# Kernel tuning notes

Measured on AMD Instinct MI355X. Metric: run time of the kernel, lower is better.

Reference implementation:

```python
import jax, jax.numpy as jnp
import numpy as np

jax.config.update("jax_enable_x64", True)  # hash arithmetic needs 64-bit ints

P = 56598313          # RzLinear.P (prime for the hash)
INPUT_DIM = 4096
OUTPUT_DIM = 4096
COMPRESS_RATIO = 0.0625
HASH_SIZE = int(INPUT_DIM * OUTPUT_DIM * COMPRESS_RATIO)  # 1,048,576
N_TOKENS = 8192


def setup_inputs() -> dict:
    key = jax.random.key(0)
    kx, kw, kr = jax.random.split(key, 3)
    x = jax.random.normal(kx, (N_TOKENS, INPUT_DIM), dtype=jnp.float32)
    hashed_weight = jax.random.normal(kw, (HASH_SIZE,), dtype=jnp.float32) * 0.02
    # _generate_random_numbers: [P, r1, r2, r3] with r_i forced even via r + r % 2
    r = jax.random.randint(kr, (3,), 0, P, dtype=jnp.int64)
    r = r + r % 2
    random_numbers = jnp.concatenate([jnp.array([P], dtype=jnp.int64), r])
    bias = jnp.zeros((OUTPUT_DIM,), dtype=jnp.float32)
    return {"x": x, "hashed_weight": hashed_weight,
            "random_numbers": random_numbers, "bias": bias}


def _hash_indices(random_numbers):
    # ROBE-Z hash (chunk_size=1): idx[k, n] = ((k*r3 + n*r2 + r1) % P) % HASH_SIZE
    r0 = random_numbers[0]
    r1 = random_numbers[1]
    r2 = random_numbers[2]
    r3 = random_numbers[3]
    k = jnp.arange(INPUT_DIM, dtype=jnp.int64)[:, None]   # (K, 1)
    n = jnp.arange(OUTPUT_DIM, dtype=jnp.int64)[None, :]  # (1, N)
    return ((k * r3 + n * r2 + r1) % r0) % HASH_SIZE       # (K, N)


def reference(x, hashed_weight, random_numbers, bias):
    idx = _hash_indices(random_numbers)
    W = hashed_weight[idx]          # gather-reconstructed (input_dim, output_dim)
    return x @ W + bias             # (N_TOKENS, output_dim)
```

## Files before the change

kernel.cpp:

```cpp
#include <hip/hip_runtime.h>
#include <stdint.h>


#define P_CONST 56598313u
#define HASH_MASK 0xFFFFFu
#define M_DIM 8192
#define N_DIM 4096
#define K_DIM 4096
#define BK 32
#define KSTEPS (K_DIM / BK)

typedef __attribute__((ext_vector_type(8))) short bf16x8;
typedef __attribute__((ext_vector_type(4))) float f32x4;

__device__ __forceinline__ unsigned short f2bf(float f) {
    unsigned int u = __float_as_uint(f);
    return (unsigned short)((u + 0x7FFFu + ((u >> 16) & 1u)) >> 16);
}

struct RN { unsigned long long r1, r2, r3; };

__device__ __forceinline__ RN decode_rn(const void* rn_raw) {
    RN o;
    const long long* rn64 = (const long long*)rn_raw;
    if (rn64[0] == 56598313LL) {
        o.r1 = (unsigned long long)rn64[1];
        o.r2 = (unsigned long long)rn64[2];
        o.r3 = (unsigned long long)rn64[3];
    } else {
        const int* rn32 = (const int*)rn_raw;
        o.r1 = (unsigned long long)(unsigned int)rn32[1];
        o.r2 = (unsigned long long)(unsigned int)rn32[2];
        o.r3 = (unsigned long long)(unsigned int)rn32[3];
    }
    return o;
}

__device__ __forceinline__ void load16(const void* g, void* l) {
    __builtin_amdgcn_global_load_lds(
        (const __attribute__((address_space(1))) void*)g,
        (__attribute__((address_space(3))) void*)l,
        16, 0, 0);
}

__global__ __launch_bounds__(256) void build_wt(const float* __restrict__ table,
                                                const void* __restrict__ rn_raw,
                                                unsigned short* __restrict__ Wt) {
    RN rn = decode_rn(rn_raw);
    const unsigned int stepu = (unsigned int)(rn.r3 % P_CONST);
    const unsigned int n = blockIdx.x;
    const unsigned long long base =
        ((unsigned long long)n * rn.r2 + rn.r1) % P_CONST;
    const int t = threadIdx.x;
#pragma unroll
    for (int e = 0; e < 2; ++e) {
        const int k0 = (t + e * 256) * 8;
        unsigned int cur =
            (unsigned int)((base + (unsigned long long)k0 * stepu) % P_CONST);
        union { unsigned short s[8]; uint4 v; } o;
#pragma unroll
        for (int i = 0; i < 8; ++i) {
            o.s[i] = f2bf(table[cur & HASH_MASK]);
            cur += stepu;
            if (cur >= P_CONST) cur -= P_CONST;
        }
        *(uint4*)(Wt + (size_t)n * K_DIM + k0) = o.v;
    }
}

__global__ __launch_bounds__(256) void cvt_x(const float* __restrict__ x,
                                             unsigned short* __restrict__ xb) {
    const size_t i8 = ((size_t)blockIdx.x * 256 + threadIdx.x) * 8;
    const float4 a = *(const float4*)(x + i8);
    const float4 b = *(const float4*)(x + i8 + 4);
    union { unsigned short s[8]; uint4 v; } o;
    o.s[0] = f2bf(a.x); o.s[1] = f2bf(a.y); o.s[2] = f2bf(a.z); o.s[3] = f2bf(a.w);
    o.s[4] = f2bf(b.x); o.s[5] = f2bf(b.y); o.s[6] = f2bf(b.z); o.s[7] = f2bf(b.w);
    *(uint4*)(xb + i8) = o.v;
}

__global__ __launch_bounds__(512, 2) void gemm_bt8(
    const unsigned short* __restrict__ A,
    const unsigned short* __restrict__ Bt,
    const float* __restrict__ bias,
    float* __restrict__ C) {
    __shared__ __align__(16) unsigned short lA[4][256 * BK];
    __shared__ __align__(16) unsigned short lB[4][256 * BK];

    const int t = threadIdx.x;
    const int bid0 = blockIdx.x;
    const int sb = (bid0 & 7) * 64 + (bid0 >> 3);
    const int m0 = (sb >> 4) * 256;
    const int n0 = (sb & 15) * 256;

    const int lane = t & 63;
    const int wid = t >> 6;
    const int wr = wid >> 2;
    const int wc = wid & 3;
    const int lm = lane & 15;
    const int q = lane >> 4;
    const int qswz = (q ^ ((lm >> 1) & 3)) << 4;

    const int p0 = t * 16;
    const int p1 = p0 + 8192;
    const int l0 = p0 ^ ((p0 >> 3) & 0x30);
    const int l1 = p1 ^ ((p1 >> 3) & 0x30);
    const int r0 = l0 >> 6, c0 = (l0 & 63) >> 1;
    const int r1 = l1 >> 6, c1 = (l1 & 63) >> 1;

    const unsigned short* Abase = A + (size_t)m0 * K_DIM;
    const unsigned short* Bbase = Bt + (size_t)n0 * K_DIM;

    f32x4 acc[8][4] = {};

#define STAGE_A(KS) do { const int b__ = (KS) & 3;                              \
    load16(Abase + (size_t)r0 * K_DIM + (KS) * BK + c0, (char*)&lA[b__][0] + p0);\
    load16(Abase + (size_t)r1 * K_DIM + (KS) * BK + c1, (char*)&lA[b__][0] + p1);\
} while (0)
#define STAGE_B(KS) do { const int b__ = (KS) & 3;                              \
    load16(Bbase + (size_t)r0 * K_DIM + (KS) * BK + c0, (char*)&lB[b__][0] + p0);\
    load16(Bbase + (size_t)r1 * K_DIM + (KS) * BK + c1, (char*)&lB[b__][0] + p1);\
} while (0)

#define STEP_BODY(KS, STG) do {                                                 \
    __builtin_amdgcn_s_barrier();                                               \
    asm volatile("" ::: "memory");                                              \
    const char* bufA = (const char*)&lA[(KS) & 3][0];                           \
    const char* bufB = (const char*)&lB[(KS) & 3][0];                           \
    bf16x8 af[4], bfr[4];                                                       \
    _Pragma("unroll")                                                           \
    for (int i = 0; i < 4; ++i)                                                 \
        af[i] = *(const bf16x8*)(bufA + (((wr * 128 + i * 16 + lm) << 6) | qswz));\
    _Pragma("unroll")                                                           \
    for (int j = 0; j < 4; ++j)                                                 \
        bfr[j] = *(const bf16x8*)(bufB + (((wc * 64 + j * 16 + lm) << 6) | qswz));\
    if (STG) STAGE_A((KS) + 3);                                                 \
    asm volatile("s_waitcnt lgkmcnt(0)" ::: "memory");                          \
    __builtin_amdgcn_sched_barrier(0);                                          \
    __builtin_amdgcn_s_setprio(1);                                              \
    _Pragma("unroll")                                                           \
    for (int i = 0; i < 4; ++i)                                                 \
        _Pragma("unroll")                                                       \
        for (int j = 0; j < 4; ++j)                                             \
            acc[i][j] = __builtin_amdgcn_mfma_f32_16x16x32_bf16(                \
                af[i], bfr[j], acc[i][j], 0, 0, 0);                             \
    __builtin_amdgcn_s_setprio(0);                                              \
    __builtin_amdgcn_s_barrier();                                               \
    asm volatile("" ::: "memory");                                              \
    _Pragma("unroll")                                                           \
    for (int i = 0; i < 4; ++i)                                                 \
        af[i] = *(const bf16x8*)(bufA + (((wr * 128 + 64 + i * 16 + lm) << 6) | qswz));\
    if (STG) STAGE_B((KS) + 3);                                                 \
    asm volatile("s_waitcnt lgkmcnt(0)" ::: "memory");                          \
    __builtin_amdgcn_sched_barrier(0);                                          \
    __builtin_amdgcn_s_setprio(1);                                              \
    _Pragma("unroll")                                                           \
    for (int i = 0; i < 4; ++i)                                                 \
        _Pragma("unroll")                                                       \
        for (int j = 0; j < 4; ++j)                                             \
            acc[i + 4][j] = __builtin_amdgcn_mfma_f32_16x16x32_bf16(            \
                af[i], bfr[j], acc[i + 4][j], 0, 0, 0);                         \
    __builtin_amdgcn_s_setprio(0);                                              \
} while (0)

    STAGE_A(0); STAGE_B(0);
    STAGE_A(1); STAGE_B(1);
    STAGE_A(2); STAGE_B(2);

#pragma unroll 1
    for (int ks = 0; ks < KSTEPS - 2; ++ks) {
        asm volatile("s_waitcnt vmcnt(8)" ::: "memory");
        STEP_BODY(ks, (ks < KSTEPS - 3));
    }
    asm volatile("s_waitcnt vmcnt(4)" ::: "memory");
    STEP_BODY(KSTEPS - 2, false);
    asm volatile("s_waitcnt vmcnt(0)" ::: "memory");
    STEP_BODY(KSTEPS - 1, false);

#undef STEP_BODY
#undef STAGE_A
#undef STAGE_B

#pragma unroll
    for (int j = 0; j < 4; ++j) {
        const int col = n0 + wc * 64 + j * 16 + lm;
        const float bv = bias[col];
#pragma unroll
        for (int i = 0; i < 8; ++i) {
            const int row = m0 + wr * 128 + i * 16 + q * 4;
#pragma unroll
            for (int r = 0; r < 4; ++r)
                C[(size_t)(row + r) * N_DIM + col] = acc[i][j][r] + bv;
        }
    }
}

__global__ __launch_bounds__(256) void gemm_fused(const float* __restrict__ X,
                                                  const float* __restrict__ table,
                                                  const void* __restrict__ rn_raw,
                                                  const float* __restrict__ bias,
                                                  float* __restrict__ C) {
    RN rn = decode_rn(rn_raw);
    const unsigned int stepu = (unsigned int)(rn.r3 % P_CONST);
    const unsigned int step32 =
        (unsigned int)(((unsigned long long)stepu * 32ull) % P_CONST);

    __shared__ __align__(16) unsigned short lA[128 * 32];
    __shared__ __align__(16) unsigned short lB[128 * 32];
    const int t = threadIdx.x;
    const int m0 = blockIdx.y * 128;
    const int n0 = blockIdx.x * 128;
    const int lane = t & 63;
    const int w = t >> 6;
    const int wr = w >> 1, wc = w & 1;
    const int lm = lane & 15, q = lane >> 4;

    unsigned int curB[2];
    int rowB[2], colB[2];
#pragma unroll
    for (int e = 0; e < 2; ++e) {
        const int c = t + e * 256;
        rowB[e] = c >> 2;
        colB[e] = (c & 3) * 8;
        const unsigned long long base =
            ((unsigned long long)(n0 + rowB[e]) * rn.r2 + rn.r1) % P_CONST;
        curB[e] =
            (unsigned int)((base + (unsigned long long)colB[e] * stepu) % P_CONST);
    }

    f32x4 acc[4][4] = {};

    for (int k0 = 0; k0 < K_DIM; k0 += 32) {
#pragma unroll
        for (int c = t; c < 1024; c += 256) {
            const int row = c >> 3, col = (c & 7) * 4;
            const float4 v =
                *(const float4*)(X + (size_t)(m0 + row) * K_DIM + k0 + col);
            ushort4 o;
            o.x = f2bf(v.x); o.y = f2bf(v.y); o.z = f2bf(v.z); o.w = f2bf(v.w);
            *(ushort4*)&lA[row * 32 + col] = o;
        }
#pragma unroll
        for (int e = 0; e < 2; ++e) {
            unsigned int cur = curB[e];
            union { unsigned short s[8]; uint4 v; } o;
#pragma unroll
            for (int i = 0; i < 8; ++i) {
                o.s[i] = f2bf(table[cur & HASH_MASK]);
                cur += stepu;
                if (cur >= P_CONST) cur -= P_CONST;
            }
            curB[e] += step32;
            if (curB[e] >= P_CONST) curB[e] -= P_CONST;
            *(uint4*)&lB[rowB[e] * 32 + colB[e]] = o.v;
        }
        __syncthreads();

        bf16x8 af[4], bfr[4];
#pragma unroll
        for (int i = 0; i < 4; ++i)
            af[i] = *(const bf16x8*)&lA[(wr * 64 + i * 16 + lm) * 32 + q * 8];
#pragma unroll
        for (int j = 0; j < 4; ++j)
            bfr[j] = *(const bf16x8*)&lB[(wc * 64 + j * 16 + lm) * 32 + q * 8];
#pragma unroll
        for (int i = 0; i < 4; ++i)
#pragma unroll
            for (int j = 0; j < 4; ++j)
                acc[i][j] = __builtin_amdgcn_mfma_f32_16x16x32_bf16(
                    af[i], bfr[j], acc[i][j], 0, 0, 0);
        __syncthreads();
    }

#pragma unroll
    for (int j = 0; j < 4; ++j) {
        const int col = n0 + wc * 64 + j * 16 + lm;
        const float bv = bias[col];
#pragma unroll
        for (int i = 0; i < 4; ++i) {
            const int row = m0 + wr * 64 + i * 16 + q * 4;
#pragma unroll
            for (int r = 0; r < 4; ++r)
                C[(size_t)(row + r) * N_DIM + col] = acc[i][j][r] + bv;
        }
    }
}

extern "C" void kernel_launch(void* const* d_in, const int* in_sizes, int n_in,
                              void* d_out, int out_size, void* d_ws, size_t ws_size,
                              hipStream_t stream) {
    const float* x = (const float*)d_in[0];
    const float* hw = (const float*)d_in[1];
    const void* rn = d_in[2];
    const float* bias = (const float*)d_in[3];
    float* out = (float*)d_out;

    const size_t wt_bytes = (size_t)N_DIM * K_DIM * 2;
    const size_t xb_bytes = (size_t)M_DIM * K_DIM * 2;

    if (ws_size >= wt_bytes + xb_bytes) {
        unsigned short* Wt = (unsigned short*)d_ws;
        unsigned short* Xb = (unsigned short*)((char*)d_ws + wt_bytes);
        build_wt<<<N_DIM, 256, 0, stream>>>(hw, rn, Wt);
        cvt_x<<<(M_DIM * K_DIM) / (8 * 256), 256, 0, stream>>>(x, Xb);
        gemm_bt8<<<dim3((M_DIM / 256) * (N_DIM / 256)), 512, 0, stream>>>(Xb, Wt, bias, out);
    } else {
        gemm_fused<<<dim3(N_DIM / 128, M_DIM / 128), 256, 0, stream>>>(x, hw, rn, bias, out);
    }
}
```

Measured before the change: 534.7 us.

## Fuse weight gather with x conversion and pre-convert hash table to bf16

The hash table is converted to bf16 once, which halves its footprint so it stays cache-resident. The weight-gather kernel and the x-to-bf16 conversion are merged into one launch, with each thread gathering four weight entries and converting eight x values. The streaming x reads and the Xb/Wt writes use nontemporal hints. This adds one small kernel and extra workspace, and falls back to an fp32-table fused prep when the workspace is too small.

```diff
diff --git a/kernel.cpp b/kernel.cpp
--- a/kernel.cpp
+++ b/kernel.cpp
@@ -12,6 +12,8 @@
 
 typedef __attribute__((ext_vector_type(8))) short bf16x8;
 typedef __attribute__((ext_vector_type(4))) float f32x4;
+typedef __attribute__((ext_vector_type(4))) unsigned int u32x4;
+typedef __attribute__((ext_vector_type(2))) unsigned int u32x2;
 
 __device__ __forceinline__ unsigned short f2bf(float f) {
     unsigned int u = __float_as_uint(f);
@@ -43,40 +45,87 @@
         16, 0, 0);
 }
 
-__global__ __launch_bounds__(256) void build_wt(const float* __restrict__ table,
-                                                const void* __restrict__ rn_raw,
-                                                unsigned short* __restrict__ Wt) {
+__global__ __launch_bounds__(256) void cvt_tbl(const float* __restrict__ table,
+                                               unsigned short* __restrict__ tb) {
+    const size_t i8 = ((size_t)blockIdx.x * 256 + threadIdx.x) * 8;
+    const f32x4 a = *(const f32x4*)(table + i8);
+    const f32x4 c = *(const f32x4*)(table + i8 + 4);
+    union { unsigned short s[8]; u32x4 v; } o;
+    o.s[0] = f2bf(a.x); o.s[1] = f2bf(a.y); o.s[2] = f2bf(a.z); o.s[3] = f2bf(a.w);
+    o.s[4] = f2bf(c.x); o.s[5] = f2bf(c.y); o.s[6] = f2bf(c.z); o.s[7] = f2bf(c.w);
+    *(u32x4*)(tb + i8) = o.v;
+}
+
+__global__ __launch_bounds__(256) void prep_bf(const float* __restrict__ x,
+                                               const unsigned short* __restrict__ tb,
+                                               const void* __restrict__ rn_raw,
+                                               unsigned short* __restrict__ Wt,
+                                               unsigned short* __restrict__ Xb) {
+    const int b = blockIdx.x;
+    const int t = threadIdx.x;
     RN rn = decode_rn(rn_raw);
     const unsigned int stepu = (unsigned int)(rn.r3 % P_CONST);
-    const unsigned int n = blockIdx.x;
+    const unsigned int n = (unsigned int)(b >> 2);
+    const int kb = ((b & 3) << 10) + (t << 2);
     const unsigned long long base =
         ((unsigned long long)n * rn.r2 + rn.r1) % P_CONST;
+    unsigned int cur =
+        (unsigned int)((base + (unsigned long long)kb * stepu) % P_CONST);
+    const unsigned int i0 = cur & HASH_MASK;
+    cur += stepu; if (cur >= P_CONST) cur -= P_CONST;
+    const unsigned int i1 = cur & HASH_MASK;
+    cur += stepu; if (cur >= P_CONST) cur -= P_CONST;
+    const unsigned int i2 = cur & HASH_MASK;
+    cur += stepu; if (cur >= P_CONST) cur -= P_CONST;
+    const unsigned int i3 = cur & HASH_MASK;
+    const unsigned short g0 = tb[i0];
+    const unsigned short g1 = tb[i1];
+    const unsigned short g2 = tb[i2];
+    const unsigned short g3 = tb[i3];
+    const size_t i8 = ((size_t)b * 256 + t) * 8;
+    const f32x4 a = __builtin_nontemporal_load((const f32x4*)(x + i8));
+    const f32x4 c = __builtin_nontemporal_load((const f32x4*)(x + i8 + 4));
+    union { unsigned short s[8]; u32x4 v; } o;
+    o.s[0] = f2bf(a.x); o.s[1] = f2bf(a.y); o.s[2] = f2bf(a.z); o.s[3] = f2bf(a.w);
+    o.s[4] = f2bf(c.x); o.s[5] = f2bf(c.y); o.s[6] = f2bf(c.z); o.s[7] = f2bf(c.w);
+    __builtin_nontemporal_store(o.v, (u32x4*)(Xb + i8));
+    union { unsigned short s[4]; u32x2 v; } w;
+    w.s[0] = g0; w.s[1] = g1; w.s[2] = g2; w.s[3] = g3;
+    __builtin_nontemporal_store(w.v, (u32x2*)(Wt + (size_t)n * K_DIM + kb));
+}
+
+__global__ __launch_bounds__(256) void prep_f32(const float* __restrict__ x,
+                                                const float* __restrict__ table,
+                                                const void* __restrict__ rn_raw,
+                                                unsigned short* __restrict__ Wt,
+                                                unsigned short* __restrict__ Xb) {
+    const int b = blockIdx.x;
     const int t = threadIdx.x;
-#pragma unroll
-    for (int e = 0; e < 2; ++e) {
-        const int k0 = (t + e * 256) * 8;
-        unsigned int cur =
-            (unsigned int)((base + (unsigned long long)k0 * stepu) % P_CONST);
-        union { unsigned short s[8]; uint4 v; } o;
-#pragma unroll
-        for (int i = 0; i < 8; ++i) {
-            o.s[i] = f2bf(table[cur & HASH_MASK]);
-            cur += stepu;
-            if (cur >= P_CONST) cur -= P_CONST;
-        }
-        *(uint4*)(Wt + (size_t)n * K_DIM + k0) = o.v;
-    }
-}
-
-__global__ __launch_bounds__(256) void cvt_x(const float* __restrict__ x,
-                                             unsigned short* __restrict__ xb) {
-    const size_t i8 = ((size_t)blockIdx.x * 256 + threadIdx.x) * 8;
-    const float4 a = *(const float4*)(x + i8);
-    const float4 b = *(const float4*)(x + i8 + 4);
-    union { unsigned short s[8]; uint4 v; } o;
+    RN rn = decode_rn(rn_raw);
+    const unsigned int stepu = (unsigned int)(rn.r3 % P_CONST);
+    const unsigned int n = (unsigned int)(b >> 2);
+    const int kb = ((b & 3) << 10) + (t << 2);
+    const unsigned long long base =
+        ((unsigned long long)n * rn.r2 + rn.r1) % P_CONST;
+    unsigned int cur =
+        (unsigned int)((base + (unsigned long long)kb * stepu) % P_CONST);
+    const float g0 = table[cur & HASH_MASK];
+    cur += stepu; if (cur >= P_CONST) cur -= P_CONST;
+    const float g1 = table[cur & HASH_MASK];
+    cur += stepu; if (cur >= P_CONST) cur -= P_CONST;
+    const float g2 = table[cur & HASH_MASK];
+    cur += stepu; if (cur >= P_CONST) cur -= P_CONST;
+    const float g3 = table[cur & HASH_MASK];
+    const size_t i8 = ((size_t)b * 256 + t) * 8;
+    const f32x4 a = __builtin_nontemporal_load((const f32x4*)(x + i8));
+    const f32x4 c = __builtin_nontemporal_load((const f32x4*)(x + i8 + 4));
+    union { unsigned short s[8]; u32x4 v; } o;
     o.s[0] = f2bf(a.x); o.s[1] = f2bf(a.y); o.s[2] = f2bf(a.z); o.s[3] = f2bf(a.w);
-    o.s[4] = f2bf(b.x); o.s[5] = f2bf(b.y); o.s[6] = f2bf(b.z); o.s[7] = f2bf(b.w);
-    *(uint4*)(xb + i8) = o.v;
+    o.s[4] = f2bf(c.x); o.s[5] = f2bf(c.y); o.s[6] = f2bf(c.z); o.s[7] = f2bf(c.w);
+    __builtin_nontemporal_store(o.v, (u32x4*)(Xb + i8));
+    union { unsigned short s[4]; u32x2 v; } w;
+    w.s[0] = f2bf(g0); w.s[1] = f2bf(g1); w.s[2] = f2bf(g2); w.s[3] = f2bf(g3);
+    __builtin_nontemporal_store(w.v, (u32x2*)(Wt + (size_t)n * K_DIM + kb));
 }
 
 __global__ __launch_bounds__(512, 2) void gemm_bt8(
@@ -297,12 +346,19 @@
 
     const size_t wt_bytes = (size_t)N_DIM * K_DIM * 2;
     const size_t xb_bytes = (size_t)M_DIM * K_DIM * 2;
-
-    if (ws_size >= wt_bytes + xb_bytes) {
+    const size_t tb_bytes = (size_t)(HASH_MASK + 1) * 2;
+
+    if (ws_size >= wt_bytes + xb_bytes + tb_bytes) {
         unsigned short* Wt = (unsigned short*)d_ws;
         unsigned short* Xb = (unsigned short*)((char*)d_ws + wt_bytes);
-        build_wt<<<N_DIM, 256, 0, stream>>>(hw, rn, Wt);
-        cvt_x<<<(M_DIM * K_DIM) / (8 * 256), 256, 0, stream>>>(x, Xb);
+        unsigned short* Tb = (unsigned short*)((char*)d_ws + wt_bytes + xb_bytes);
+        cvt_tbl<<<512, 256, 0, stream>>>(hw, Tb);
+        prep_bf<<<16384, 256, 0, stream>>>(x, Tb, rn, Wt, Xb);
+        gemm_bt8<<<dim3((M_DIM / 256) * (N_DIM / 256)), 512, 0, stream>>>(Xb, Wt, bias, out);
+    } else if (ws_size >= wt_bytes + xb_bytes) {
+        unsigned short* Wt = (unsigned short*)d_ws;
+        unsigned short* Xb = (unsigned short*)((char*)d_ws + wt_bytes);
+        prep_f32<<<16384, 256, 0, stream>>>(x, hw, rn, Wt, Xb);
         gemm_bt8<<<dim3((M_DIM / 256) * (N_DIM / 256)), 512, 0, stream>>>(Xb, Wt, bias, out);
     } else {
         gemm_fused<<<dim3(N_DIM / 128, M_DIM / 128), 256, 0, stream>>>(x, hw, rn, bias, out);
```

Result: slower. 571.1 us (+6.8%).

## Build hashed weight via bf16 table staged through LDS shards

Applied to the files above, without the earlier changes.

Converts the hash table to bf16 once, then rebuilds the weight matrix with 1024-thread blocks that stream the table through a 128KB LDS buffer in 16 shards. Each thread gathers its entries from LDS and keeps only those whose index falls in the current shard. This replaces random global-memory gathers with coalesced loads plus LDS lookups. In exchange it adds an extra kernel launch and redundant per-shard hash and LDS work, and the single large-LDS block per CU limits occupancy.

```diff
diff --git a/kernel.cpp b/kernel.cpp
--- a/kernel.cpp
+++ b/kernel.cpp
@@ -12,6 +12,7 @@
 
 typedef __attribute__((ext_vector_type(8))) short bf16x8;
 typedef __attribute__((ext_vector_type(4))) float f32x4;
+typedef __attribute__((ext_vector_type(4))) unsigned int u32x4;
 
 __device__ __forceinline__ unsigned short f2bf(float f) {
     unsigned int u = __float_as_uint(f);
@@ -43,6 +44,78 @@
         16, 0, 0);
 }
 
+__global__ __launch_bounds__(256) void cvt_tbl(const float* __restrict__ table,
+                                               unsigned short* __restrict__ tb) {
+    const size_t i8 = ((size_t)blockIdx.x * 256 + threadIdx.x) * 8;
+    const f32x4 a = *(const f32x4*)(table + i8);
+    const f32x4 c = *(const f32x4*)(table + i8 + 4);
+    union { unsigned short s[8]; u32x4 v; } o;
+    o.s[0] = f2bf(a.x); o.s[1] = f2bf(a.y); o.s[2] = f2bf(a.z); o.s[3] = f2bf(a.w);
+    o.s[4] = f2bf(c.x); o.s[5] = f2bf(c.y); o.s[6] = f2bf(c.z); o.s[7] = f2bf(c.w);
+    *(u32x4*)(tb + i8) = o.v;
+}
+
+__global__ __launch_bounds__(1024) void build_wt_lds(
+    const unsigned short* __restrict__ tb,
+    const void* __restrict__ rn_raw,
+    unsigned short* __restrict__ Wt) {
+    __shared__ __align__(16) unsigned short shard[65536];
+    RN rn = decode_rn(rn_raw);
+    const unsigned int stepu = (unsigned int)(rn.r3 % P_CONST);
+    const unsigned int jump504 =
+        (unsigned int)((504ull * stepu) % P_CONST);
+    const int b = blockIdx.x;
+    const int t = threadIdx.x;
+    const unsigned int n = (unsigned int)(b * 16 + (t >> 6));
+    const int kbase = (t & 63) * 8;
+    const unsigned long long base =
+        ((unsigned long long)n * rn.r2 + rn.r1) % P_CONST;
+    const unsigned int cur0 =
+        (unsigned int)((base + (unsigned long long)kbase * stepu) % P_CONST);
+
+    bf16x8 wv[8] = {};
+
+#pragma unroll 1
+    for (int s = 0; s < 16; ++s) {
+        __syncthreads();
+#pragma unroll
+        for (int i = 0; i < 8; ++i)
+            load16(tb + ((size_t)s << 16) + (i << 13) + t * 8,
+                   (char*)shard + (i << 14) + t * 16);
+        asm volatile("s_waitcnt vmcnt(0)" ::: "memory");
+        __syncthreads();
+
+        unsigned int cur = cur0;
+#pragma unroll
+        for (int j = 0; j < 8; ++j) {
+#pragma unroll
+            for (int i = 0; i < 8; ++i) {
+                const unsigned int idx = cur & HASH_MASK;
+                const unsigned short v = shard[idx & 0xFFFFu];
+                if ((idx >> 16) == (unsigned int)s) wv[j][i] = (short)v;
+                cur += stepu; if (cur >= P_CONST) cur -= P_CONST;
+            }
+            cur += jump504; if (cur >= P_CONST) cur -= P_CONST;
+        }
+    }
+
+    unsigned short* dst = Wt + (size_t)n * K_DIM + kbase;
+#pragma unroll
+    for (int j = 0; j < 8; ++j)
+        *(bf16x8*)(dst + j * 512) = wv[j];
+}
+
+__global__ __launch_bounds__(256) void cvt_x(const float* __restrict__ x,
+                                             unsigned short* __restrict__ xb) {
+    const size_t i8 = ((size_t)blockIdx.x * 256 + threadIdx.x) * 8;
+    const f32x4 a = *(const f32x4*)(x + i8);
+    const f32x4 c = *(const f32x4*)(x + i8 + 4);
+    union { unsigned short s[8]; u32x4 v; } o;
+    o.s[0] = f2bf(a.x); o.s[1] = f2bf(a.y); o.s[2] = f2bf(a.z); o.s[3] = f2bf(a.w);
+    o.s[4] = f2bf(c.x); o.s[5] = f2bf(c.y); o.s[6] = f2bf(c.z); o.s[7] = f2bf(c.w);
+    *(u32x4*)(xb + i8) = o.v;
+}
+
 __global__ __launch_bounds__(256) void build_wt(const float* __restrict__ table,
                                                 const void* __restrict__ rn_raw,
                                                 unsigned short* __restrict__ Wt) {
@@ -57,26 +130,15 @@
         const int k0 = (t + e * 256) * 8;
         unsigned int cur =
             (unsigned int)((base + (unsigned long long)k0 * stepu) % P_CONST);
-        union { unsigned short s[8]; uint4 v; } o;
+        union { unsigned short s[8]; u32x4 v; } o;
 #pragma unroll
         for (int i = 0; i < 8; ++i) {
             o.s[i] = f2bf(table[cur & HASH_MASK]);
             cur += stepu;
             if (cur >= P_CONST) cur -= P_CONST;
         }
-        *(uint4*)(Wt + (size_t)n * K_DIM + k0) = o.v;
-    }
-}
-
-__global__ __launch_bounds__(256) void cvt_x(const float* __restrict__ x,
-                                             unsigned short* __restrict__ xb) {
-    const size_t i8 = ((size_t)blockIdx.x * 256 + threadIdx.x) * 8;
-    const float4 a = *(const float4*)(x + i8);
-    const float4 b = *(const float4*)(x + i8 + 4);
-    union { unsigned short s[8]; uint4 v; } o;
-    o.s[0] = f2bf(a.x); o.s[1] = f2bf(a.y); o.s[2] = f2bf(a.z); o.s[3] = f2bf(a.w);
-    o.s[4] = f2bf(b.x); o.s[5] = f2bf(b.y); o.s[6] = f2bf(b.z); o.s[7] = f2bf(b.w);
-    *(uint4*)(xb + i8) = o.v;
+        *(u32x4*)(Wt + (size_t)n * K_DIM + k0) = o.v;
+    }
 }
 
 __global__ __launch_bounds__(512, 2) void gemm_bt8(
@@ -297,8 +359,17 @@
 
     const size_t wt_bytes = (size_t)N_DIM * K_DIM * 2;
     const size_t xb_bytes = (size_t)M_DIM * K_DIM * 2;
-
-    if (ws_size >= wt_bytes + xb_bytes) {
+    const size_t tb_bytes = (size_t)(HASH_MASK + 1) * 2;
+
+    if (ws_size >= wt_bytes + xb_bytes + tb_bytes) {
+        unsigned short* Wt = (unsigned short*)d_ws;
+        unsigned short* Xb = (unsigned short*)((char*)d_ws + wt_bytes);
+        unsigned short* Tb = (unsigned short*)((char*)d_ws + wt_bytes + xb_bytes);
+        cvt_tbl<<<512, 256, 0, stream>>>(hw, Tb);
+        build_wt_lds<<<256, 1024, 0, stream>>>(Tb, rn, Wt);
+        cvt_x<<<(M_DIM * K_DIM) / (8 * 256), 256, 0, stream>>>(x, Xb);
+        gemm_bt8<<<dim3((M_DIM / 256) * (N_DIM / 256)), 512, 0, stream>>>(Xb, Wt, bias, out);
+    } else if (ws_size >= wt_bytes + xb_bytes) {
         unsigned short* Wt = (unsigned short*)d_ws;
         unsigned short* Xb = (unsigned short*)((char*)d_ws + wt_bytes);
         build_wt<<<N_DIM, 256, 0, stream>>>(hw, rn, Wt);
```

Result: slower. 763.5 us (+42.8%).
